# Performance work log

Measured on AMD Instinct MI355X. Metric: run time of the kernel, lower is better.

## Reference

```python
import jax, jax.numpy as jnp
import numpy as np

# Static per-expert capacities (tokens are laid out contiguously per expert)
CAPS = [1024, 512, 1024, 256, 1024, 512, 128, 1024, 512, 1024, 256, 512, 1024, 128, 64, 512]
TOTAL = sum(CAPS)  # 9536
E, H, I = 16, 1024, 4096
OFFSETS = np.concatenate([[0], np.cumsum(CAPS)])


def setup_inputs() -> dict:
    key = jax.random.key(0)
    ks = jax.random.split(key, 5)
    x = jax.random.normal(ks[0], (TOTAL, H), dtype=jnp.float32)
    W1 = jax.random.normal(ks[1], (E, I, H), dtype=jnp.float32) * 0.02
    b1 = jax.random.normal(ks[2], (E, I), dtype=jnp.float32) * 0.02
    W2 = jax.random.normal(ks[3], (E, H, I), dtype=jnp.float32) * 0.02
    b2 = jax.random.normal(ks[4], (E, H), dtype=jnp.float32) * 0.02
    return {"x": x, "W1": W1, "b1": b1, "W2": W2, "b2": b2}


def reference(x, W1, b1, W2, b2):
    # Grouped GEMM FFN: expert e processes rows [OFFSETS[e]:OFFSETS[e+1]]
    # out = gelu(x_e @ W1[e].T + b1[e]) @ W2[e].T + b2[e]
    outs = []
    for e in range(E):  # fixed, static loop over experts (capacities are static)
        xs = x[OFFSETS[e]:OFFSETS[e + 1]]                      # [cap_e, H]
        h = jax.nn.gelu(xs @ W1[e].T + b1[e], approximate=False)  # [cap_e, I]
        outs.append(h @ W2[e].T + b2[e])                       # [cap_e, H]
    return jnp.concatenate(outs, axis=0)                       # [TOTAL, H]
```

## Files before the change

### kernel.cpp

```cpp
#include <hip/hip_runtime.h>
#include <math.h>

typedef __attribute__((ext_vector_type(8))) short short8;
typedef __attribute__((ext_vector_type(4))) float f32x4;
typedef __attribute__((ext_vector_type(2))) unsigned int u32x2;
typedef __attribute__((ext_vector_type(4))) unsigned int u32x4;

#define E_NUM 16
constexpr int CAPS[E_NUM] = {1024,512,1024,256,1024,512,128,1024,512,1024,256,512,1024,128,64,512};
constexpr int OFFS[E_NUM] = {0,1024,1536,2560,2816,3840,4352,4480,5504,6016,7040,7296,7808,8832,8960,9024};
constexpr int cdiv_(int a, int b){ return (a + b - 1) / b; }
constexpr int ilog2_(int v){ int l = 0; while ((1 << l) < v) ++l; return l; }

__device__ __forceinline__ unsigned int cvt_pk_bf16(float a, float b){
  unsigned int r;
  asm("v_cvt_pk_bf16_f32 %0, %1, %2" : "=v"(r) : "v"(a), "v"(b));
  return r;
}

typedef __attribute__((address_space(1))) const unsigned char gas_u8;
typedef __attribute__((address_space(3))) unsigned char las_u8;
__device__ __forceinline__ void gl_lds16(const void* g, void* l){
  __builtin_amdgcn_global_load_lds((gas_u8*)g, (las_u8*)l, 16, 0, 0);
}

__global__ __launch_bounds__(256) void cvt_bf16_kernel(const float* __restrict__ x,
                                                       unsigned short* __restrict__ xb, int n8)
{
  int i = blockIdx.x * blockDim.x + threadIdx.x;
  const int stride = gridDim.x * blockDim.x;
  for (; i < n8; i += stride) {
    f32x4 a = *reinterpret_cast<const f32x4*>(x + (size_t)i * 8);
    f32x4 b = *reinterpret_cast<const f32x4*>(x + (size_t)i * 8 + 4);
    u32x2 lo, hi;
    lo[0] = cvt_pk_bf16(a[0], a[1]); lo[1] = cvt_pk_bf16(a[2], a[3]);
    hi[0] = cvt_pk_bf16(b[0], b[1]); hi[1] = cvt_pk_bf16(b[2], b[3]);
    *reinterpret_cast<u32x2*>(xb + (size_t)i * 8)     = lo;
    *reinterpret_cast<u32x2*>(xb + (size_t)i * 8 + 4) = hi;
  }
}

template<bool A_BF16, bool GELU_OUT, int NDIM, int KDIM, int LOG_GN, int NWG, int KS>
__global__ __launch_bounds__(512, 2)
void expert_gemm256(const void* __restrict__ Av, const float* __restrict__ W,
                    const float* __restrict__ bias, void* __restrict__ Outv)
{
  constexpr int A_BYTES = 256 * 64;
  constexpr int B_BYTES = 256 * 128;
  constexpr int BUF  = A_BYTES + B_BYTES;
  constexpr int NBUF = A_BF16 ? 3 : 2;
  constexpr int GN   = 1 << LOG_GN;
  constexpr int NTT  = KDIM / (KS * 32);
  constexpr int NWG1 = NWG / KS;
  static_assert(NWG % 8 == 0, "grid must be divisible by 8 for XCD swizzle");
  static_assert(NTT >= 3, "pipeline needs >=3 K-steps");

  __shared__ __align__(16) char smem[NBUF * BUF];

  const int tid  = threadIdx.x;
  const int braw = blockIdx.x;
  const int t = (braw & 7) * (NWG / 8) + (braw >> 3);

  const int kc    = t / NWG1;
  const int tt    = t % NWG1;
  const int kbase = kc * (KDIM / KS);

  int m0 = 0, n0 = 0, Me = 0, tok0 = 0;
  size_t wbase = 0, bbase = 0;
  {
    int acc0 = 0;
    #pragma unroll
    for (int i = 0; i < E_NUM; ++i) {
      const int mt  = cdiv_(CAPS[i], 256);
      const int lmt = ilog2_(mt);
      const int nb  = mt * (NDIM / 256);
      if (tt >= acc0 && tt < acc0 + nb) {
        const int loc = tt - acc0;
        const int g   = loc >> (lmt + LOG_GN);
        const int rem = loc & ((mt << LOG_GN) - 1);
        m0   = (rem >> LOG_GN) * 256;
        n0   = ((g << LOG_GN) | (rem & (GN - 1))) * 256;
        Me   = CAPS[i];
        tok0 = OFFS[i];
        wbase = (size_t)i * NDIM * KDIM;
        bbase = (size_t)i * NDIM;
      }
      acc0 += nb;
    }
  }
  const float* Wb = W + wbase;

  const int lane = tid & 63;
  const int wv   = tid >> 6;

  const unsigned short* Ah = (const unsigned short*)Av;
  const float*          Af = (const float*)Av;

  auto stageA = [&](int buf, int kt) {
    const unsigned short* Ag = Ah + (size_t)(tok0 + m0) * KDIM + kbase + kt * 32;
    char* dst0 = smem + buf * BUF;
    #pragma unroll
    for (int j = 0; j < 2; ++j) {
      const int rbase = j * 128 + wv * 16;
      const int r     = rbase + (lane >> 2);
      const int blk   = (lane & 3) ^ (r & 3);
      gl_lds16((const void*)(Ag + (size_t)r * KDIM + blk * 8), (void*)(dst0 + rbase * 64));
    }
  };
  auto stageB = [&](int buf, int kt) {
    const float* Bg = Wb + (size_t)n0 * KDIM + kbase + kt * 32;
    char* dst0 = smem + buf * BUF + A_BYTES;
    #pragma unroll
    for (int j = 0; j < 4; ++j) {
      const int rbase = j * 64 + wv * 8;
      const int r     = rbase + (lane >> 3);
      const int blk   = (lane & 7) ^ (r & 7);
      gl_lds16((const void*)(Bg + (size_t)r * KDIM + blk * 4), (void*)(dst0 + rbase * 128));
    }
  };

  const int fr = tid >> 1;
  const int fcq = (tid & 1) * 2;
  f32x4 raf[4];
  auto loadA_reg = [&](int kt) {
    const float* Ap = Af + (size_t)(tok0 + m0 + fr) * KDIM + kbase + kt * 32 + fcq * 8;
    #pragma unroll
    for (int i = 0; i < 4; ++i)
      raf[i] = *reinterpret_cast<const f32x4*>(Ap + i * 4);
  };
  auto writeA_reg = [&](int buf) {
    char* ab = smem + buf * BUF;
    #pragma unroll
    for (int i = 0; i < 2; ++i) {
      u32x2 p;
      p[0] = cvt_pk_bf16(raf[2*i][0], raf[2*i][1]);
      p[1] = cvt_pk_bf16(raf[2*i][2], raf[2*i][3]);
      const int blk = (fcq + i) ^ (fr & 3);
      *reinterpret_cast<u32x2*>(ab + fr * 64 + blk * 16) = p;
    }
  };

  const int wm   = (wv >> 2) * 128;
  const int wn   = (wv & 3) * 64;
  const int lrow = lane & 15;
  const int pa0  = (((lane >> 4) ^ (lane & 3)) << 4);
  const int pb0  = ((((lane >> 4) << 1) ^ (lane & 7)) << 4);

  f32x4 acc_[8][4];
  #pragma unroll
  for (int i = 0; i < 8; ++i)
    #pragma unroll
    for (int j = 0; j < 4; ++j)
      acc_[i][j] = (f32x4){0.f, 0.f, 0.f, 0.f};

  auto compute = [&](int cur) {
    const char* ab  = smem + cur * BUF;
    const char* bbp = smem + cur * BUF + A_BYTES;
    short8 bfr[4];
    #pragma unroll
    for (int f = 0; f < 4; ++f) {
      const char* rowp = bbp + (size_t)(wn + f * 16 + lrow) * 128;
      f32x4 lo = *reinterpret_cast<const f32x4*>(rowp + pb0);
      f32x4 hi = *reinterpret_cast<const f32x4*>(rowp + (pb0 ^ 16));
      u32x4 pk;
      pk[0] = cvt_pk_bf16(lo[0], lo[1]); pk[1] = cvt_pk_bf16(lo[2], lo[3]);
      pk[2] = cvt_pk_bf16(hi[0], hi[1]); pk[3] = cvt_pk_bf16(hi[2], hi[3]);
      bfr[f] = __builtin_bit_cast(short8, pk);
    }
    #pragma unroll
    for (int i = 0; i < 8; ++i) {
      short8 afr = *reinterpret_cast<const short8*>(ab + (wm + i * 16 + lrow) * 64 + pa0);
      #pragma unroll
      for (int j = 0; j < 4; ++j)
        acc_[i][j] = __builtin_amdgcn_mfma_f32_16x16x32_bf16(afr, bfr[j], acc_[i][j], 0, 0, 0);
    }
  };

  if constexpr (A_BF16) {
    stageA(0, 0); stageB(0, 0);
    stageA(1, 1); stageB(1, 1);
    int cur = 0, nx2 = 2;
    for (int kt = 0; kt < NTT; ++kt) {
      if (kt + 1 < NTT) {
        asm volatile("s_waitcnt vmcnt(6)\n\ts_barrier" ::: "memory");
      } else {
        asm volatile("s_waitcnt vmcnt(0)\n\ts_barrier" ::: "memory");
      }
      __builtin_amdgcn_sched_barrier(0);
      if (kt + 2 < NTT) { stageA(nx2, kt + 2); stageB(nx2, kt + 2); }
      compute(cur);
      cur = (cur == 2) ? 0 : cur + 1;
      nx2 = (nx2 == 2) ? 0 : nx2 + 1;
    }
  } else {
    loadA_reg(0); stageB(0, 0); writeA_reg(0);
    __syncthreads();
    for (int kt = 0; kt < NTT; ++kt) {
      const int cur = kt & 1;
      if (kt + 1 < NTT) { stageB(cur ^ 1, kt + 1); loadA_reg(kt + 1); }
      compute(cur);
      if (kt + 1 < NTT) writeA_reg(cur ^ 1);
      __syncthreads();
    }
  }

  float bv[4];
  #pragma unroll
  for (int f = 0; f < 4; ++f)
    bv[f] = bias[bbase + n0 + wn + f * 16 + lrow];

  if constexpr (GELU_OUT) {
    unsigned short* Oh = (unsigned short*)Outv;
    if constexpr (A_BF16) {
      __syncthreads();
      unsigned short* hout = (unsigned short*)smem;
      #pragma unroll
      for (int i = 0; i < 8; ++i) {
        const int rbase = wm + i * 16 + (lane >> 4) * 4;
        #pragma unroll
        for (int j = 0; j < 4; ++j) {
          #pragma unroll
          for (int jj = 0; jj < 4; ++jj) {
            float xv = acc_[i][j][jj] + bv[j];
            float y2 = xv * (1.5957691216057308f + 0.07135481627f * xv * xv);
            float g  = xv * __builtin_amdgcn_rcpf(1.0f + __expf(-y2));
            hout[(rbase + jj) * 256 + wn + j * 16 + lrow] = (unsigned short)(cvt_pk_bf16(g, g) & 0xFFFFu);
          }
        }
      }
      __syncthreads();
      #pragma unroll
      for (int s = 0; s < 16; ++s) {
        const int row = s * 16 + (tid >> 5);
        const int c   = (tid & 31) * 8;
        if (m0 + row < Me) {
          *reinterpret_cast<short8*>(Oh + (size_t)(tok0 + m0 + row) * NDIM + n0 + c)
            = *reinterpret_cast<const short8*>(hout + row * 256 + c);
        }
      }
    } else {
      #pragma unroll
      for (int i = 0; i < 8; ++i) {
        const int rbase = wm + i * 16 + (lane >> 4) * 4;
        #pragma unroll
        for (int j = 0; j < 4; ++j) {
          #pragma unroll
          for (int jj = 0; jj < 4; ++jj) {
            int grow = m0 + rbase + jj;
            if (grow < Me) {
              float xv = acc_[i][j][jj] + bv[j];
              float y2 = xv * (1.5957691216057308f + 0.07135481627f * xv * xv);
              float g  = xv * __builtin_amdgcn_rcpf(1.0f + __expf(-y2));
              Oh[(size_t)(tok0 + grow) * NDIM + n0 + wn + j * 16 + lrow]
                = (unsigned short)(cvt_pk_bf16(g, g) & 0xFFFFu);
            }
          }
        }
      }
    }
  } else {
    float* Of = (float*)Outv;
    constexpr float BS = 1.0f / (float)KS;
    #pragma unroll
    for (int i = 0; i < 8; ++i) {
      const int rbase = wm + i * 16 + (lane >> 4) * 4;
      #pragma unroll
      for (int jj = 0; jj < 4; ++jj) {
        int grow = m0 + rbase + jj;
        if (grow < Me) {
          #pragma unroll
          for (int j = 0; j < 4; ++j) {
            float v = acc_[i][j][jj] + bv[j] * BS;
            float* p = Of + (size_t)(tok0 + grow) * NDIM + n0 + wn + j * 16 + lrow;
            if constexpr (KS > 1) unsafeAtomicAdd(p, v);
            else                  *p = v;
          }
        }
      }
    }
  }
}

extern "C" void kernel_launch(void* const* d_in, const int* in_sizes, int n_in,
                              void* d_out, int out_size, void* d_ws, size_t ws_size,
                              hipStream_t stream)
{
  const float* x  = (const float*)d_in[0];
  const float* W1 = (const float*)d_in[1];
  const float* b1 = (const float*)d_in[2];
  const float* W2 = (const float*)d_in[3];
  const float* b2 = (const float*)d_in[4];
  float* out = (float*)d_out;

  constexpr size_t H_BYTES  = (size_t)9536 * 4096 * 2;
  constexpr size_t XB_BYTES = (size_t)9536 * 1024 * 2;
  unsigned short* h  = (unsigned short*)d_ws;
  unsigned short* xb = (unsigned short*)((char*)d_ws + H_BYTES);

  const bool use_xb = ws_size >= H_BYTES + XB_BYTES;

  hipMemsetAsync(d_out, 0, (size_t)out_size * sizeof(float), stream);

  if (use_xb) {
    cvt_bf16_kernel<<<2048, 256, 0, stream>>>(x, xb, 9536 * 1024 / 8);
    expert_gemm256<true, true, 4096, 1024, 2, 624, 1>
        <<<624, 512, 0, stream>>>((const void*)xb, W1, b1, (void*)h);
  } else {
    expert_gemm256<false, true, 4096, 1024, 2, 624, 1>
        <<<624, 512, 0, stream>>>((const void*)x, W1, b1, (void*)h);
  }

  expert_gemm256<true, false, 1024, 4096, 2, 624, 4>
      <<<624, 512, 0, stream>>>((const void*)h, W2, b2, (void*)out);
}
```

Before: 398.0 us.

## Replace second GEMM with 128x128-tile kernel using split-K of 2

After: 368.5 us. 7.4% less time.

```diff
diff --git a/kernel.cpp b/kernel.cpp
--- a/kernel.cpp
+++ b/kernel.cpp
@@ -40,30 +40,25 @@
   }
 }
 
-template<bool A_BF16, bool GELU_OUT, int NDIM, int KDIM, int LOG_GN, int NWG, int KS>
+template<bool A_BF16, int NDIM, int KDIM, int LOG_GN, int NWG>
 __global__ __launch_bounds__(512, 2)
-void expert_gemm256(const void* __restrict__ Av, const float* __restrict__ W,
-                    const float* __restrict__ bias, void* __restrict__ Outv)
+void g1_gemm256(const void* __restrict__ Av, const float* __restrict__ W,
+                const float* __restrict__ bias, void* __restrict__ Outv)
 {
   constexpr int A_BYTES = 256 * 64;
   constexpr int B_BYTES = 256 * 128;
   constexpr int BUF  = A_BYTES + B_BYTES;
   constexpr int NBUF = A_BF16 ? 3 : 2;
   constexpr int GN   = 1 << LOG_GN;
-  constexpr int NTT  = KDIM / (KS * 32);
-  constexpr int NWG1 = NWG / KS;
-  static_assert(NWG % 8 == 0, "grid must be divisible by 8 for XCD swizzle");
-  static_assert(NTT >= 3, "pipeline needs >=3 K-steps");
+  constexpr int NTT  = KDIM / 32;
+  static_assert(NWG % 8 == 0);
+  static_assert(NTT >= 3);
 
   __shared__ __align__(16) char smem[NBUF * BUF];
 
   const int tid  = threadIdx.x;
   const int braw = blockIdx.x;
-  const int t = (braw & 7) * (NWG / 8) + (braw >> 3);
-
-  const int kc    = t / NWG1;
-  const int tt    = t % NWG1;
-  const int kbase = kc * (KDIM / KS);
+  const int tt = (braw & 7) * (NWG / 8) + (braw >> 3);
 
   int m0 = 0, n0 = 0, Me = 0, tok0 = 0;
   size_t wbase = 0, bbase = 0;
@@ -97,7 +92,7 @@
   const float*          Af = (const float*)Av;
 
   auto stageA = [&](int buf, int kt) {
-    const unsigned short* Ag = Ah + (size_t)(tok0 + m0) * KDIM + kbase + kt * 32;
+    const unsigned short* Ag = Ah + (size_t)(tok0 + m0) * KDIM + kt * 32;
     char* dst0 = smem + buf * BUF;
     #pragma unroll
     for (int j = 0; j < 2; ++j) {
@@ -108,7 +103,7 @@
     }
   };
   auto stageB = [&](int buf, int kt) {
-    const float* Bg = Wb + (size_t)n0 * KDIM + kbase + kt * 32;
+    const float* Bg = Wb + (size_t)n0 * KDIM + kt * 32;
     char* dst0 = smem + buf * BUF + A_BYTES;
     #pragma unroll
     for (int j = 0; j < 4; ++j) {
@@ -123,10 +118,9 @@
   const int fcq = (tid & 1) * 2;
   f32x4 raf[4];
   auto loadA_reg = [&](int kt) {
-    const float* Ap = Af + (size_t)(tok0 + m0 + fr) * KDIM + kbase + kt * 32 + fcq * 8;
-    #pragma unroll
-    for (int i = 0; i < 4; ++i)
-      raf[i] = *reinterpret_cast<const f32x4*>(Ap + i * 4);
+    const float* Ap = Af + (size_t)(tok0 + m0 + fr) * KDIM + kt * 32 + fcq * 8;
+    #pragma unroll
+    for (int i = 0; i < 4; ++i) raf[i] = *reinterpret_cast<const f32x4*>(Ap + i * 4);
   };
   auto writeA_reg = [&](int buf) {
     char* ab = smem + buf * BUF;
@@ -181,11 +175,8 @@
     stageA(1, 1); stageB(1, 1);
     int cur = 0, nx2 = 2;
     for (int kt = 0; kt < NTT; ++kt) {
-      if (kt + 1 < NTT) {
-        asm volatile("s_waitcnt vmcnt(6)\n\ts_barrier" ::: "memory");
-      } else {
-        asm volatile("s_waitcnt vmcnt(0)\n\ts_barrier" ::: "memory");
-      }
+      if (kt + 1 < NTT) asm volatile("s_waitcnt vmcnt(6)\n\ts_barrier" ::: "memory");
+      else              asm volatile("s_waitcnt vmcnt(0)\n\ts_barrier" ::: "memory");
       __builtin_amdgcn_sched_barrier(0);
       if (kt + 2 < NTT) { stageA(nx2, kt + 2); stageB(nx2, kt + 2); }
       compute(cur);
@@ -209,72 +200,198 @@
   for (int f = 0; f < 4; ++f)
     bv[f] = bias[bbase + n0 + wn + f * 16 + lrow];
 
-  if constexpr (GELU_OUT) {
-    unsigned short* Oh = (unsigned short*)Outv;
-    if constexpr (A_BF16) {
-      __syncthreads();
-      unsigned short* hout = (unsigned short*)smem;
+  unsigned short* Oh = (unsigned short*)Outv;
+  if constexpr (A_BF16) {
+    __syncthreads();
+    unsigned short* hout = (unsigned short*)smem;
+    #pragma unroll
+    for (int i = 0; i < 8; ++i) {
+      const int rbase = wm + i * 16 + (lane >> 4) * 4;
       #pragma unroll
-      for (int i = 0; i < 8; ++i) {
-        const int rbase = wm + i * 16 + (lane >> 4) * 4;
+      for (int j = 0; j < 4; ++j) {
         #pragma unroll
-        for (int j = 0; j < 4; ++j) {
-          #pragma unroll
-          for (int jj = 0; jj < 4; ++jj) {
+        for (int jj = 0; jj < 4; ++jj) {
+          float xv = acc_[i][j][jj] + bv[j];
+          float y2 = xv * (1.5957691216057308f + 0.07135481627f * xv * xv);
+          float g  = xv * __builtin_amdgcn_rcpf(1.0f + __expf(-y2));
+          hout[(rbase + jj) * 256 + wn + j * 16 + lrow] = (unsigned short)(cvt_pk_bf16(g, g) & 0xFFFFu);
+        }
+      }
+    }
+    __syncthreads();
+    #pragma unroll
+    for (int s = 0; s < 16; ++s) {
+      const int row = s * 16 + (tid >> 5);
+      const int c   = (tid & 31) * 8;
+      if (m0 + row < Me) {
+        *reinterpret_cast<short8*>(Oh + (size_t)(tok0 + m0 + row) * NDIM + n0 + c)
+          = *reinterpret_cast<const short8*>(hout + row * 256 + c);
+      }
+    }
+  } else {
+    #pragma unroll
+    for (int i = 0; i < 8; ++i) {
+      const int rbase = wm + i * 16 + (lane >> 4) * 4;
+      #pragma unroll
+      for (int j = 0; j < 4; ++j) {
+        #pragma unroll
+        for (int jj = 0; jj < 4; ++jj) {
+          int grow = m0 + rbase + jj;
+          if (grow < Me) {
             float xv = acc_[i][j][jj] + bv[j];
             float y2 = xv * (1.5957691216057308f + 0.07135481627f * xv * xv);
             float g  = xv * __builtin_amdgcn_rcpf(1.0f + __expf(-y2));
-            hout[(rbase + jj) * 256 + wn + j * 16 + lrow] = (unsigned short)(cvt_pk_bf16(g, g) & 0xFFFFu);
+            Oh[(size_t)(tok0 + grow) * NDIM + n0 + wn + j * 16 + lrow]
+              = (unsigned short)(cvt_pk_bf16(g, g) & 0xFFFFu);
           }
         }
       }
-      __syncthreads();
+    }
+  }
+}
+
+template<int NDIM, int KDIM, int LOG_GN, int NWG, int KS>
+__global__ __launch_bounds__(256, 8)
+void g2_gemm128(const unsigned short* __restrict__ Ah, const float* __restrict__ W,
+                const float* __restrict__ bias, float* __restrict__ Of)
+{
+  constexpr int A_BYTES = 128 * 64;
+  constexpr int B_BYTES = 128 * 64;
+  constexpr int GN   = 1 << LOG_GN;
+  constexpr int NT   = KDIM / (KS * 32);
+  constexpr int NWG1 = NWG / KS;
+  static_assert(NWG % 8 == 0);
+
+  __shared__ __align__(16) char smem[2 * A_BYTES + 2 * B_BYTES];
+
+  const int tid  = threadIdx.x;
+  const int braw = blockIdx.x;
+  const int t = (braw & 7) * (NWG / 8) + (braw >> 3);
+
+  const int kc    = t / NWG1;
+  const int tt    = t % NWG1;
+  const int kbase = kc * (KDIM / KS);
+
+  int m0 = 0, n0 = 0, Me = 0, tok0 = 0;
+  size_t wbase = 0, bbase = 0;
+  {
+    int acc0 = 0;
+    #pragma unroll
+    for (int i = 0; i < E_NUM; ++i) {
+      const int mt  = cdiv_(CAPS[i], 128);
+      const int lmt = ilog2_(mt);
+      const int nb  = mt * (NDIM / 128);
+      if (tt >= acc0 && tt < acc0 + nb) {
+        const int loc = tt - acc0;
+        const int g   = loc >> (lmt + LOG_GN);
+        const int rem = loc & ((mt << LOG_GN) - 1);
+        m0   = (rem >> LOG_GN) * 128;
+        n0   = ((g << LOG_GN) | (rem & (GN - 1))) * 128;
+        Me   = CAPS[i];
+        tok0 = OFFS[i];
+        wbase = (size_t)i * NDIM * KDIM;
+        bbase = (size_t)i * NDIM;
+      }
+      acc0 += nb;
+    }
+  }
+  const float* Wb = W + wbase;
+
+  const int lane = tid & 63;
+  const int wv   = tid >> 6;
+  const int sr   = tid >> 3;
+  const int sc   = (tid & 7) * 8;
+  const int spc  = sc ^ (((sr >> 2) & 3) << 4);
+
+  f32x4 rb[4];
+  auto loadB = [&](int kt) {
+    const int k0 = kbase + kt * 32;
+    #pragma unroll
+    for (int i = 0; i < 4; ++i)
+      rb[i] = *reinterpret_cast<const f32x4*>(Wb + (size_t)(n0 + sr + 32 * i) * KDIM + k0 + (sc >> 1));
+  };
+  auto writeB = [&](int buf) {
+    char* bb = smem + 2 * A_BYTES + buf * B_BYTES;
+    #pragma unroll
+    for (int i = 0; i < 4; ++i) {
+      u32x2 p;
+      p[0] = cvt_pk_bf16(rb[i][0], rb[i][1]);
+      p[1] = cvt_pk_bf16(rb[i][2], rb[i][3]);
+      *reinterpret_cast<u32x2*>(bb + (sr + 32 * i) * 64 + spc) = p;
+    }
+  };
+
+  auto stageA = [&](int buf, int kt) {
+    const unsigned short* Ag = Ah + (size_t)(tok0 + m0) * KDIM + kbase + kt * 32;
+    char* dst0 = smem + buf * A_BYTES;
+    #pragma unroll
+    for (int j = 0; j < 2; ++j) {
+      const int rbase = wv * 32 + j * 16;
+      const int r     = rbase + (lane >> 2);
+      const int blk   = (lane & 3) ^ ((r >> 2) & 3);
+      gl_lds16((const void*)(Ag + (size_t)r * KDIM + blk * 8), (void*)(dst0 + rbase * 64));
+    }
+  };
+
+  const int wm   = (wv >> 1) * 64;
+  const int wn   = (wv & 1) * 64;
+  const int lrow = lane & 15;
+  const int fcs  = ((lane >> 4) << 4) ^ (((lane >> 2) & 3) << 4);
+
+  f32x4 acc_[4][4];
+  #pragma unroll
+  for (int i = 0; i < 4; ++i)
+    #pragma unroll
+    for (int j = 0; j < 4; ++j)
+      acc_[i][j] = (f32x4){0.f, 0.f, 0.f, 0.f};
+
+  auto mfma_step = [&](int cur) {
+    const char* ab = smem + cur * A_BYTES;
+    const char* bb = smem + 2 * A_BYTES + cur * B_BYTES;
+    short8 afr[4], bfr[4];
+    #pragma unroll
+    for (int f = 0; f < 4; ++f)
+      afr[f] = *reinterpret_cast<const short8*>(ab + (wm + f * 16 + lrow) * 64 + fcs);
+    #pragma unroll
+    for (int f = 0; f < 4; ++f)
+      bfr[f] = *reinterpret_cast<const short8*>(bb + (wn + f * 16 + lrow) * 64 + fcs);
+    #pragma unroll
+    for (int i = 0; i < 4; ++i)
       #pragma unroll
-      for (int s = 0; s < 16; ++s) {
-        const int row = s * 16 + (tid >> 5);
-        const int c   = (tid & 31) * 8;
-        if (m0 + row < Me) {
-          *reinterpret_cast<short8*>(Oh + (size_t)(tok0 + m0 + row) * NDIM + n0 + c)
-            = *reinterpret_cast<const short8*>(hout + row * 256 + c);
-        }
-      }
-    } else {
-      #pragma unroll
-      for (int i = 0; i < 8; ++i) {
-        const int rbase = wm + i * 16 + (lane >> 4) * 4;
+      for (int j = 0; j < 4; ++j)
+        acc_[i][j] = __builtin_amdgcn_mfma_f32_16x16x32_bf16(afr[i], bfr[j], acc_[i][j], 0, 0, 0);
+  };
+
+  loadB(0); stageA(0, 0); writeB(0);
+  __syncthreads();
+
+  for (int kt = 0; kt < NT; ++kt) {
+    const int cur = kt & 1;
+    if (kt + 1 < NT) { loadB(kt + 1); stageA(cur ^ 1, kt + 1); }
+    mfma_step(cur);
+    if (kt + 1 < NT) writeB(cur ^ 1);
+    __syncthreads();
+  }
+
+  float bv[4];
+  #pragma unroll
+  for (int f = 0; f < 4; ++f)
+    bv[f] = bias[bbase + n0 + wn + f * 16 + lrow];
+
+  constexpr float BS = 1.0f / (float)KS;
+  #pragma unroll
+  for (int i = 0; i < 4; ++i) {
+    const int rbase = wm + i * 16 + (lane >> 4) * 4;
+    #pragma unroll
+    for (int jj = 0; jj < 4; ++jj) {
+      int grow = m0 + rbase + jj;
+      if (grow < Me) {
         #pragma unroll
         for (int j = 0; j < 4; ++j) {
-          #pragma unroll
-          for (int jj = 0; jj < 4; ++jj) {
-            int grow = m0 + rbase + jj;
-            if (grow < Me) {
-              float xv = acc_[i][j][jj] + bv[j];
-              float y2 = xv * (1.5957691216057308f + 0.07135481627f * xv * xv);
-              float g  = xv * __builtin_amdgcn_rcpf(1.0f + __expf(-y2));
-              Oh[(size_t)(tok0 + grow) * NDIM + n0 + wn + j * 16 + lrow]
-                = (unsigned short)(cvt_pk_bf16(g, g) & 0xFFFFu);
-            }
-          }
-        }
-      }
-    }
-  } else {
-    float* Of = (float*)Outv;
-    constexpr float BS = 1.0f / (float)KS;
-    #pragma unroll
-    for (int i = 0; i < 8; ++i) {
-      const int rbase = wm + i * 16 + (lane >> 4) * 4;
-      #pragma unroll
-      for (int jj = 0; jj < 4; ++jj) {
-        int grow = m0 + rbase + jj;
-        if (grow < Me) {
-          #pragma unroll
-          for (int j = 0; j < 4; ++j) {
-            float v = acc_[i][j][jj] + bv[j] * BS;
-            float* p = Of + (size_t)(tok0 + grow) * NDIM + n0 + wn + j * 16 + lrow;
-            if constexpr (KS > 1) unsafeAtomicAdd(p, v);
-            else                  *p = v;
-          }
+          float v = acc_[i][j][jj] + bv[j] * BS;
+          float* p = Of + (size_t)(tok0 + grow) * NDIM + n0 + wn + j * 16 + lrow;
+          if constexpr (KS > 1) unsafeAtomicAdd(p, v);
+          else                  *p = v;
         }
       }
     }
@@ -303,13 +420,13 @@
 
   if (use_xb) {
     cvt_bf16_kernel<<<2048, 256, 0, stream>>>(x, xb, 9536 * 1024 / 8);
-    expert_gemm256<true, true, 4096, 1024, 2, 624, 1>
+    g1_gemm256<true, 4096, 1024, 2, 624>
         <<<624, 512, 0, stream>>>((const void*)xb, W1, b1, (void*)h);
   } else {
-    expert_gemm256<false, true, 4096, 1024, 2, 624, 1>
+    g1_gemm256<false, 4096, 1024, 2, 624>
         <<<624, 512, 0, stream>>>((const void*)x, W1, b1, (void*)h);
   }
 
-  expert_gemm256<true, false, 1024, 4096, 2, 624, 4>
-      <<<624, 512, 0, stream>>>((const void*)h, W2, b2, (void*)out);
-}
+  g2_gemm128<1024, 4096, 2, 1200, 2>
+      <<<1200, 256, 0, stream>>>(h, W2, b2, out);
+}
```

## Overlap W2 bf16 conversion with first GEMM and run second GEMM on bf16 weights

Applied to the files above, without the earlier changes.

Measured after the change: 417.2 us. 4.8% more time.

```diff
diff --git a/kernel.cpp b/kernel.cpp
--- a/kernel.cpp
+++ b/kernel.cpp
@@ -40,30 +40,22 @@
   }
 }
 
-template<bool A_BF16, bool GELU_OUT, int NDIM, int KDIM, int LOG_GN, int NWG, int KS>
-__global__ __launch_bounds__(512, 2)
-void expert_gemm256(const void* __restrict__ Av, const float* __restrict__ W,
-                    const float* __restrict__ bias, void* __restrict__ Outv)
+template<int NDIM, int KDIM, int LOG_GN, int NWG>
+__device__ __forceinline__ void g1_body(int braw, const unsigned short* __restrict__ Ah,
+                                        const float* __restrict__ W,
+                                        const float* __restrict__ bias,
+                                        unsigned short* __restrict__ Oh, char* smem)
 {
   constexpr int A_BYTES = 256 * 64;
   constexpr int B_BYTES = 256 * 128;
   constexpr int BUF  = A_BYTES + B_BYTES;
-  constexpr int NBUF = A_BF16 ? 3 : 2;
   constexpr int GN   = 1 << LOG_GN;
-  constexpr int NTT  = KDIM / (KS * 32);
-  constexpr int NWG1 = NWG / KS;
-  static_assert(NWG % 8 == 0, "grid must be divisible by 8 for XCD swizzle");
-  static_assert(NTT >= 3, "pipeline needs >=3 K-steps");
-
-  __shared__ __align__(16) char smem[NBUF * BUF];
-
-  const int tid  = threadIdx.x;
-  const int braw = blockIdx.x;
-  const int t = (braw & 7) * (NWG / 8) + (braw >> 3);
-
-  const int kc    = t / NWG1;
-  const int tt    = t % NWG1;
-  const int kbase = kc * (KDIM / KS);
+  constexpr int NTT  = KDIM / 32;
+  static_assert(NWG % 8 == 0);
+  static_assert(NTT >= 3);
+
+  const int tid = threadIdx.x;
+  const int tt = (braw & 7) * (NWG / 8) + (braw >> 3);
 
   int m0 = 0, n0 = 0, Me = 0, tok0 = 0;
   size_t wbase = 0, bbase = 0;
@@ -93,11 +85,8 @@
   const int lane = tid & 63;
   const int wv   = tid >> 6;
 
-  const unsigned short* Ah = (const unsigned short*)Av;
-  const float*          Af = (const float*)Av;
-
   auto stageA = [&](int buf, int kt) {
-    const unsigned short* Ag = Ah + (size_t)(tok0 + m0) * KDIM + kbase + kt * 32;
+    const unsigned short* Ag = Ah + (size_t)(tok0 + m0) * KDIM + kt * 32;
     char* dst0 = smem + buf * BUF;
     #pragma unroll
     for (int j = 0; j < 2; ++j) {
@@ -108,7 +97,7 @@
     }
   };
   auto stageB = [&](int buf, int kt) {
-    const float* Bg = Wb + (size_t)n0 * KDIM + kbase + kt * 32;
+    const float* Bg = Wb + (size_t)n0 * KDIM + kt * 32;
     char* dst0 = smem + buf * BUF + A_BYTES;
     #pragma unroll
     for (int j = 0; j < 4; ++j) {
@@ -116,27 +105,6 @@
       const int r     = rbase + (lane >> 3);
       const int blk   = (lane & 7) ^ (r & 7);
       gl_lds16((const void*)(Bg + (size_t)r * KDIM + blk * 4), (void*)(dst0 + rbase * 128));
-    }
-  };
-
-  const int fr = tid >> 1;
-  const int fcq = (tid & 1) * 2;
-  f32x4 raf[4];
-  auto loadA_reg = [&](int kt) {
-    const float* Ap = Af + (size_t)(tok0 + m0 + fr) * KDIM + kbase + kt * 32 + fcq * 8;
-    #pragma unroll
-    for (int i = 0; i < 4; ++i)
-      raf[i] = *reinterpret_cast<const f32x4*>(Ap + i * 4);
-  };
-  auto writeA_reg = [&](int buf) {
-    char* ab = smem + buf * BUF;
-    #pragma unroll
-    for (int i = 0; i < 2; ++i) {
-      u32x2 p;
-      p[0] = cvt_pk_bf16(raf[2*i][0], raf[2*i][1]);
-      p[1] = cvt_pk_bf16(raf[2*i][2], raf[2*i][3]);
-      const int blk = (fcq + i) ^ (fr & 3);
-      *reinterpret_cast<u32x2*>(ab + fr * 64 + blk * 16) = p;
     }
   };
 
@@ -176,32 +144,17 @@
     }
   };
 
-  if constexpr (A_BF16) {
-    stageA(0, 0); stageB(0, 0);
-    stageA(1, 1); stageB(1, 1);
-    int cur = 0, nx2 = 2;
-    for (int kt = 0; kt < NTT; ++kt) {
-      if (kt + 1 < NTT) {
-        asm volatile("s_waitcnt vmcnt(6)\n\ts_barrier" ::: "memory");
-      } else {
-        asm volatile("s_waitcnt vmcnt(0)\n\ts_barrier" ::: "memory");
-      }
-      __builtin_amdgcn_sched_barrier(0);
-      if (kt + 2 < NTT) { stageA(nx2, kt + 2); stageB(nx2, kt + 2); }
-      compute(cur);
-      cur = (cur == 2) ? 0 : cur + 1;
-      nx2 = (nx2 == 2) ? 0 : nx2 + 1;
-    }
-  } else {
-    loadA_reg(0); stageB(0, 0); writeA_reg(0);
-    __syncthreads();
-    for (int kt = 0; kt < NTT; ++kt) {
-      const int cur = kt & 1;
-      if (kt + 1 < NTT) { stageB(cur ^ 1, kt + 1); loadA_reg(kt + 1); }
-      compute(cur);
-      if (kt + 1 < NTT) writeA_reg(cur ^ 1);
-      __syncthreads();
-    }
+  stageA(0, 0); stageB(0, 0);
+  stageA(1, 1); stageB(1, 1);
+  int cur = 0, nx2 = 2;
+  for (int kt = 0; kt < NTT; ++kt) {
+    if (kt + 1 < NTT) asm volatile("s_waitcnt vmcnt(6)\n\ts_barrier" ::: "memory");
+    else              asm volatile("s_waitcnt vmcnt(0)\n\ts_barrier" ::: "memory");
+    __builtin_amdgcn_sched_barrier(0);
+    if (kt + 2 < NTT) { stageA(nx2, kt + 2); stageB(nx2, kt + 2); }
+    compute(cur);
+    cur = (cur == 2) ? 0 : cur + 1;
+    nx2 = (nx2 == 2) ? 0 : nx2 + 1;
   }
 
   float bv[4];
@@ -209,72 +162,183 @@
   for (int f = 0; f < 4; ++f)
     bv[f] = bias[bbase + n0 + wn + f * 16 + lrow];
 
-  if constexpr (GELU_OUT) {
-    unsigned short* Oh = (unsigned short*)Outv;
-    if constexpr (A_BF16) {
-      __syncthreads();
-      unsigned short* hout = (unsigned short*)smem;
+  __syncthreads();
+  unsigned short* hout = (unsigned short*)smem;
+  #pragma unroll
+  for (int i = 0; i < 8; ++i) {
+    const int rbase = wm + i * 16 + (lane >> 4) * 4;
+    #pragma unroll
+    for (int j = 0; j < 4; ++j) {
       #pragma unroll
-      for (int i = 0; i < 8; ++i) {
-        const int rbase = wm + i * 16 + (lane >> 4) * 4;
+      for (int jj = 0; jj < 4; ++jj) {
+        float xv = acc_[i][j][jj] + bv[j];
+        float y2 = xv * (1.5957691216057308f + 0.07135481627f * xv * xv);
+        float g  = xv * __builtin_amdgcn_rcpf(1.0f + __expf(-y2));
+        hout[(rbase + jj) * 256 + wn + j * 16 + lrow] = (unsigned short)(cvt_pk_bf16(g, g) & 0xFFFFu);
+      }
+    }
+  }
+  __syncthreads();
+  #pragma unroll
+  for (int s = 0; s < 16; ++s) {
+    const int row = s * 16 + (tid >> 5);
+    const int c   = (tid & 31) * 8;
+    if (m0 + row < Me) {
+      *reinterpret_cast<short8*>(Oh + (size_t)(tok0 + m0 + row) * NDIM + n0 + c)
+        = *reinterpret_cast<const short8*>(hout + row * 256 + c);
+    }
+  }
+}
+
+constexpr int G1_NWG  = 624;
+constexpr int CVT_NWG = 640;
+
+__global__ __launch_bounds__(512, 2)
+void g1cvt(const unsigned short* __restrict__ xb, const float* __restrict__ W1,
+           const float* __restrict__ b1, unsigned short* __restrict__ h,
+           const float* __restrict__ W2, unsigned short* __restrict__ w2b)
+{
+  __shared__ __align__(16) char smem[3 * (256 * 64 + 256 * 128)];
+  if ((int)blockIdx.x < G1_NWG) {
+    g1_body<4096, 1024, 2, G1_NWG>(blockIdx.x, xb, W1, b1, h, smem);
+  } else {
+    constexpr int N8 = 16 * 1024 * 4096 / 8;
+    int i = ((int)blockIdx.x - G1_NWG) * 512 + (int)threadIdx.x;
+    const int stride = CVT_NWG * 512;
+    for (; i < N8; i += stride) {
+      f32x4 a = *reinterpret_cast<const f32x4*>(W2 + (size_t)i * 8);
+      f32x4 b = *reinterpret_cast<const f32x4*>(W2 + (size_t)i * 8 + 4);
+      u32x2 lo, hi;
+      lo[0] = cvt_pk_bf16(a[0], a[1]); lo[1] = cvt_pk_bf16(a[2], a[3]);
+      hi[0] = cvt_pk_bf16(b[0], b[1]); hi[1] = cvt_pk_bf16(b[2], b[3]);
+      *reinterpret_cast<u32x2*>(w2b + (size_t)i * 8)     = lo;
+      *reinterpret_cast<u32x2*>(w2b + (size_t)i * 8 + 4) = hi;
+    }
+  }
+}
+
+template<int NDIM, int KDIM, int NWG, int KS>
+__global__ __launch_bounds__(512, 1)
+void g2_gemm256b(const unsigned short* __restrict__ Ah, const unsigned short* __restrict__ Wh,
+                 const float* __restrict__ bias, float* __restrict__ Of)
+{
+  constexpr int T_BYTES = 256 * 64;
+  constexpr int BUF  = 2 * T_BYTES;
+  constexpr int NT   = KDIM / (KS * 32);
+  constexpr int NWG1 = NWG / KS;
+  static_assert(NWG % 8 == 0);
+  static_assert(NT >= 3);
+
+  __shared__ __align__(16) char smem[3 * BUF];
+
+  const int tid  = threadIdx.x;
+  const int braw = blockIdx.x;
+  const int t = (braw & 7) * (NWG / 8) + (braw >> 3);
+
+  const int kc    = t / NWG1;
+  const int tt    = t % NWG1;
+  const int kbase = kc * (KDIM / KS);
+
+  int m0 = 0, n0 = 0, Me = 0, tok0 = 0;
+  size_t wbase = 0, bbase = 0;
+  {
+    int acc0 = 0;
+    #pragma unroll
+    for (int i = 0; i < E_NUM; ++i) {
+      const int mt = cdiv_(CAPS[i], 256);
+      const int nb = mt * (NDIM / 256);
+      if (tt >= acc0 && tt < acc0 + nb) {
+        const int loc = tt - acc0;
+        m0   = (loc & (mt - 1)) * 256;
+        n0   = (loc >> ilog2_(mt)) * 256;
+        Me   = CAPS[i];
+        tok0 = OFFS[i];
+        wbase = (size_t)i * NDIM * KDIM;
+        bbase = (size_t)i * NDIM;
+      }
+      acc0 += nb;
+    }
+  }
+
+  const int lane = tid & 63;
+  const int wv   = tid >> 6;
+
+  const unsigned short* Abase = Ah + (size_t)(tok0 + m0) * KDIM + kbase;
+  const unsigned short* Bbase = Wh + wbase + (size_t)n0 * KDIM + kbase;
+
+  auto stage_tile = [&](const unsigned short* base, char* dst0, int kt) {
+    const unsigned short* Tg = base + kt * 32;
+    #pragma unroll
+    for (int j = 0; j < 2; ++j) {
+      const int rbase = wv * 32 + j * 16;
+      const int r     = rbase + (lane >> 2);
+      const int blk   = (lane & 3) ^ (r & 3);
+      gl_lds16((const void*)(Tg + (size_t)r * KDIM + blk * 8), (void*)(dst0 + rbase * 64));
+    }
+  };
+  auto stage = [&](int buf, int kt) {
+    stage_tile(Abase, smem + buf * BUF, kt);
+    stage_tile(Bbase, smem + buf * BUF + T_BYTES, kt);
+  };
+
+  const int wm   = (wv >> 2) * 128;
+  const int wn   = (wv & 3) * 64;
+  const int lrow = lane & 15;
+  const int pa0  = (((lane >> 4) ^ (lane & 3)) << 4);
+
+  f32x4 acc_[8][4];
+  #pragma unroll
+  for (int i = 0; i < 8; ++i)
+    #pragma unroll
+    for (int j = 0; j < 4; ++j)
+      acc_[i][j] = (f32x4){0.f, 0.f, 0.f, 0.f};
+
+  auto compute = [&](int cur) {
+    const char* ab = smem + cur * BUF;
+    const char* bb = smem + cur * BUF + T_BYTES;
+    short8 bfr[4];
+    #pragma unroll
+    for (int f = 0; f < 4; ++f)
+      bfr[f] = *reinterpret_cast<const short8*>(bb + (wn + f * 16 + lrow) * 64 + pa0);
+    #pragma unroll
+    for (int i = 0; i < 8; ++i) {
+      short8 afr = *reinterpret_cast<const short8*>(ab + (wm + i * 16 + lrow) * 64 + pa0);
+      #pragma unroll
+      for (int j = 0; j < 4; ++j)
+        acc_[i][j] = __builtin_amdgcn_mfma_f32_16x16x32_bf16(afr, bfr[j], acc_[i][j], 0, 0, 0);
+    }
+  };
+
+  stage(0, 0);
+  stage(1, 1);
+  int cur = 0, nx2 = 2;
+  for (int kt = 0; kt < NT; ++kt) {
+    if (kt + 1 < NT) asm volatile("s_waitcnt vmcnt(4)\n\ts_barrier" ::: "memory");
+    else             asm volatile("s_waitcnt vmcnt(0)\n\ts_barrier" ::: "memory");
+    __builtin_amdgcn_sched_barrier(0);
+    if (kt + 2 < NT) stage(nx2, kt + 2);
+    compute(cur);
+    cur = (cur == 2) ? 0 : cur + 1;
+    nx2 = (nx2 == 2) ? 0 : nx2 + 1;
+  }
+
+  float bv[4];
+  #pragma unroll
+  for (int f = 0; f < 4; ++f)
+    bv[f] = bias[bbase + n0 + wn + f * 16 + lrow];
+
+  constexpr float BS = 1.0f / (float)KS;
+  #pragma unroll
+  for (int i = 0; i < 8; ++i) {
+    const int rbase = wm + i * 16 + (lane >> 4) * 4;
+    #pragma unroll
+    for (int jj = 0; jj < 4; ++jj) {
+      int grow = m0 + rbase + jj;
+      if (grow < Me) {
         #pragma unroll
         for (int j = 0; j < 4; ++j) {
-          #pragma unroll
-          for (int jj = 0; jj < 4; ++jj) {
-            float xv = acc_[i][j][jj] + bv[j];
-            float y2 = xv * (1.5957691216057308f + 0.07135481627f * xv * xv);
-            float g  = xv * __builtin_amdgcn_rcpf(1.0f + __expf(-y2));
-            hout[(rbase + jj) * 256 + wn + j * 16 + lrow] = (unsigned short)(cvt_pk_bf16(g, g) & 0xFFFFu);
-          }
-        }
-      }
-      __syncthreads();
-      #pragma unroll
-      for (int s = 0; s < 16; ++s) {
-        const int row = s * 16 + (tid >> 5);
-        const int c   = (tid & 31) * 8;
-        if (m0 + row < Me) {
-          *reinterpret_cast<short8*>(Oh + (size_t)(tok0 + m0 + row) * NDIM + n0 + c)
-            = *reinterpret_cast<const short8*>(hout + row * 256 + c);
-        }
-      }
-    } else {
-      #pragma unroll
-      for (int i = 0; i < 8; ++i) {
-        const int rbase = wm + i * 16 + (lane >> 4) * 4;
-        #pragma unroll
-        for (int j = 0; j < 4; ++j) {
-          #pragma unroll
-          for (int jj = 0; jj < 4; ++jj) {
-            int grow = m0 + rbase + jj;
-            if (grow < Me) {
-              float xv = acc_[i][j][jj] + bv[j];
-              float y2 = xv * (1.5957691216057308f + 0.07135481627f * xv * xv);
-              float g  = xv * __builtin_amdgcn_rcpf(1.0f + __expf(-y2));
-              Oh[(size_t)(tok0 + grow) * NDIM + n0 + wn + j * 16 + lrow]
-                = (unsigned short)(cvt_pk_bf16(g, g) & 0xFFFFu);
-            }
-          }
-        }
-      }
-    }
-  } else {
-    float* Of = (float*)Outv;
-    constexpr float BS = 1.0f / (float)KS;
-    #pragma unroll
-    for (int i = 0; i < 8; ++i) {
-      const int rbase = wm + i * 16 + (lane >> 4) * 4;
-      #pragma unroll
-      for (int jj = 0; jj < 4; ++jj) {
-        int grow = m0 + rbase + jj;
-        if (grow < Me) {
-          #pragma unroll
-          for (int j = 0; j < 4; ++j) {
-            float v = acc_[i][j][jj] + bv[j] * BS;
-            float* p = Of + (size_t)(tok0 + grow) * NDIM + n0 + wn + j * 16 + lrow;
-            if constexpr (KS > 1) unsafeAtomicAdd(p, v);
-            else                  *p = v;
-          }
+          float v = acc_[i][j][jj] + bv[j] * BS;
+          unsafeAtomicAdd(Of + (size_t)(tok0 + grow) * NDIM + n0 + wn + j * 16 + lrow, v);
         }
       }
     }
@@ -292,24 +356,17 @@
   const float* b2 = (const float*)d_in[4];
   float* out = (float*)d_out;
 
-  constexpr size_t H_BYTES  = (size_t)9536 * 4096 * 2;
-  constexpr size_t XB_BYTES = (size_t)9536 * 1024 * 2;
-  unsigned short* h  = (unsigned short*)d_ws;
-  unsigned short* xb = (unsigned short*)((char*)d_ws + H_BYTES);
-
-  const bool use_xb = ws_size >= H_BYTES + XB_BYTES;
+  constexpr size_t H_BYTES   = (size_t)9536 * 4096 * 2;
+  constexpr size_t XB_BYTES  = (size_t)9536 * 1024 * 2;
+  unsigned short* h   = (unsigned short*)d_ws;
+  unsigned short* xb  = (unsigned short*)((char*)d_ws + H_BYTES);
+  unsigned short* w2b = (unsigned short*)((char*)d_ws + H_BYTES + XB_BYTES);
 
   hipMemsetAsync(d_out, 0, (size_t)out_size * sizeof(float), stream);
 
-  if (use_xb) {
-    cvt_bf16_kernel<<<2048, 256, 0, stream>>>(x, xb, 9536 * 1024 / 8);
-    expert_gemm256<true, true, 4096, 1024, 2, 624, 1>
-        <<<624, 512, 0, stream>>>((const void*)xb, W1, b1, (void*)h);
-  } else {
-    expert_gemm256<false, true, 4096, 1024, 2, 624, 1>
-        <<<624, 512, 0, stream>>>((const void*)x, W1, b1, (void*)h);
-  }
-
-  expert_gemm256<true, false, 1024, 4096, 2, 624, 4>
-      <<<624, 512, 0, stream>>>((const void*)h, W2, b2, (void*)out);
-}
+  cvt_bf16_kernel<<<2048, 256, 0, stream>>>(x, xb, 9536 * 1024 / 8);
+
+  g1cvt<<<G1_NWG + CVT_NWG, 512, 0, stream>>>(xb, W1, b1, h, W2, w2b);
+
+  g2_gemm256b<1024, 4096, 624, 4><<<624, 512, 0, stream>>>(h, w2b, b2, out);
+}
```
